# Optimization experiments

Measured on AMD Instinct MI355X. Metric: run time of the kernel, lower is better.

Reference implementation:

```python
import jax, jax.numpy as jnp
import numpy as np

N, Lq, Lk = 4, 4096, 4096
H, P = 16, 128
D = H * P  # 2048


def setup_inputs() -> dict:
    key = jax.random.key(0)
    ks = jax.random.split(key, 7)
    s = 1.0 / np.sqrt(D).astype(np.float32)
    query = jax.random.normal(ks[0], (N, Lq, D), jnp.float32)
    key_t = jax.random.normal(ks[1], (N, Lk, D), jnp.float32)
    Wq = jax.random.normal(ks[2], (D, D), jnp.float32) * s
    Wk = jax.random.normal(ks[3], (D, D), jnp.float32) * s
    Wv = jax.random.normal(ks[4], (D, D), jnp.float32) * s
    query_padding_mask = jax.random.uniform(ks[5], (N, Lq)) < 0.1
    key_padding_mask = jax.random.uniform(ks[6], (N, Lk)) < 0.1
    return {"query": query, "key": key_t, "Wq": Wq, "Wk": Wk, "Wv": Wv,
            "query_padding_mask": query_padding_mask,
            "key_padding_mask": key_padding_mask}


def reference(query, key, Wq, Wk, Wv, query_padding_mask, key_padding_mask):
    n, lq, _ = query.shape
    lk = key.shape[1]
    # torch.nn.Linear(bias=False): y = x @ W^T; split into heads -> (N,H,L,P)
    q = (query @ Wq.T).reshape(n, lq, H, P).transpose(0, 2, 1, 3)
    k = (key @ Wk.T).reshape(n, lk, H, P).transpose(0, 2, 1, 3)
    v = (key @ Wv.T).reshape(n, lk, H, P).transpose(0, 2, 1, 3)
    # _log_exp_kernel(x) = log(1 + exp(x)) = softplus
    pq = jax.nn.softplus(q)
    pk = jax.nn.softplus(k)
    # zero out padded keys so they contribute nothing to numerator/denominator
    pk = jnp.where(key_padding_mask[:, None, :, None], 0.0, pk)
    # linear attention: O(L*d^2) instead of O(L^2*d)
    kv = jnp.einsum("nhkd,nhke->nhde", pk, v)          # (N,H,P,P)
    num = jnp.einsum("nhqd,nhde->nhqe", pq, kv)        # (N,H,Lq,P)
    den = jnp.einsum("nhqd,nhd->nhq", pq, pk.sum(axis=2))[..., None]
    att = num / den
    out = att.transpose(0, 2, 1, 3).reshape(n, lq, H * P)
    # zero out padded query positions
    out = jnp.where(query_padding_mask[..., None], 0.0, out)
    return out
```

## Files before the change

### kernel.cpp

```cpp
#include <hip/hip_runtime.h>
#include <stdint.h>

typedef __attribute__((ext_vector_type(8))) short    bh8;
typedef __attribute__((ext_vector_type(4))) float    fx4;
typedef __attribute__((ext_vector_type(4))) float    f4v;
typedef unsigned short u16;
typedef __attribute__((ext_vector_type(4))) unsigned short u16x4;

#define DEV static __device__ __forceinline__

DEV u16 f2bf(float f) {
  unsigned u = __float_as_uint(f);
  u += 0x7FFFu + ((u >> 16) & 1u);
  return (u16)(u >> 16);
}
DEV float bf2f(u16 s) { return __uint_as_float(((unsigned)s) << 16); }
DEV float softplus_f(float x) { return fmaxf(x, 0.f) + log1pf(expf(-fabsf(x))); }

DEV void gload_lds16(const u16* g, u16* l) {
  __builtin_amdgcn_global_load_lds(
      (const __attribute__((address_space(1))) unsigned int*)g,
      (__attribute__((address_space(3))) unsigned int*)l, 16, 0, 0);
}
DEV void stage2(const u16* s, u16* d) {
  gload_lds16(s, d);
  gload_lds16(s + 131072, d + 4096);
}

__global__ __launch_bounds__(256) void k_cvt(const float* __restrict__ in,
                                             u16* __restrict__ out, int n4) {
  int i = blockIdx.x * 256 + threadIdx.x;
  int stride = gridDim.x * 256;
  for (; i < n4; i += stride) {
    f4v v = ((const f4v*)in)[i];
    u16x4 o;
    o.x = f2bf(v.x); o.y = f2bf(v.y); o.z = f2bf(v.z); o.w = f2bf(v.w);
    ((u16x4*)out)[i] = o;
  }
}


#define MM(a, b, c) __builtin_amdgcn_mfma_f32_16x16x32_bf16(a, b, c, 0, 0, 0)
#define LD(BASE, RR, KS) \
  (*(const bh8*)&lsg[(BASE) + (RR) * 64 + ((((KS) * 32) + ko8) ^ swz)])

#define DECLQ(Q)                                                          \
  fx4 acc##Q##00 = {}, acc##Q##01 = {}, acc##Q##10 = {}, acc##Q##11 = {}, \
      acc##Q##20 = {}, acc##Q##21 = {}, acc##Q##30 = {}, acc##Q##31 = {}

#define DECLFRAGS                                                         \
  bh8 a_00 = {}, a_01 = {}, a_10 = {}, a_11 = {},                         \
      a_20 = {}, a_21 = {}, a_30 = {}, a_31 = {};                         \
  bh8 b0_00 = {}, b0_01 = {}, b0_10 = {}, b0_11 = {};                     \
  bh8 b1_00 = {}, b1_01 = {}, b1_10 = {}, b1_11 = {};

#define WV6 asm volatile("s_waitcnt vmcnt(6)");
#define WV2 asm volatile("s_waitcnt vmcnt(2)");

#define LDA4(AB, KS)                                                     \
  a_0##KS = LD(AB, arow0,      KS); a_1##KS = LD(AB, arow0 + 16, KS);    \
  a_2##KS = LD(AB, arow0 + 32, KS); a_3##KS = LD(AB, arow0 + 48, KS);

#define LDB2(BN, BB, KS)                                                 \
  b##BN##_0##KS = LD(BB, brow0,      KS);                                \
  b##BN##_1##KS = LD(BB, brow0 + 16, KS);

#define MFMA8(Q, BN, KS)                                                 \
  acc##Q##00 = MM(a_0##KS, b##BN##_0##KS, acc##Q##00);                   \
  acc##Q##01 = MM(a_0##KS, b##BN##_1##KS, acc##Q##01);                   \
  acc##Q##10 = MM(a_1##KS, b##BN##_0##KS, acc##Q##10);                   \
  acc##Q##11 = MM(a_1##KS, b##BN##_1##KS, acc##Q##11);                   \
  acc##Q##20 = MM(a_2##KS, b##BN##_0##KS, acc##Q##20);                   \
  acc##Q##21 = MM(a_2##KS, b##BN##_1##KS, acc##Q##21);                   \
  acc##Q##30 = MM(a_3##KS, b##BN##_0##KS, acc##Q##30);                   \
  acc##Q##31 = MM(a_3##KS, b##BN##_1##KS, acc##Q##31);

#define PH4(MFMAS, WAIT, ...) {                 \
  __VA_ARGS__                                   \
  __builtin_amdgcn_s_barrier();                 \
  __builtin_amdgcn_s_setprio(1);                \
  MFMAS                                         \
  __builtin_amdgcn_s_setprio(0);                \
  WAIT                                          \
  __builtin_amdgcn_s_barrier();                 \
}

#define STE(AC, EL, JOFF) {                                                   \
  float v = AC.EL;                                                            \
  if (EPI >= 1) v = softplus_f(v);                                            \
  if (EPI == 2) { if (mask[gi0 + JOFF]) v = 0.f; }                            \
  C[(size_t)(gi0 + JOFF) * 2048 + gj] = f2bf(v);                              \
}
#define ST1(AC, QR, QC, MI, NI) {                                             \
  int gi0 = bm0 + (QR) * 128 + wr * 64 + (MI) * 16 + (lane >> 4) * 4;         \
  int gj  = bn0 + (QC) * 128 + wc * 32 + (NI) * 16 + l15;                     \
  STE(AC, x, 0) STE(AC, y, 1) STE(AC, z, 2) STE(AC, w, 3)                     \
}
#define EPIQ(Q, QR, QC)                                                       \
  ST1(acc##Q##00, QR, QC, 0, 0) ST1(acc##Q##01, QR, QC, 0, 1)                 \
  ST1(acc##Q##10, QR, QC, 1, 0) ST1(acc##Q##11, QR, QC, 1, 1)                 \
  ST1(acc##Q##20, QR, QC, 2, 0) ST1(acc##Q##21, QR, QC, 2, 1)                 \
  ST1(acc##Q##30, QR, QC, 3, 0) ST1(acc##Q##31, QR, QC, 3, 1)

template <int EPI>
__global__ __launch_bounds__(512, 2) void k_gemm256(
    const u16* __restrict__ A, const u16* __restrict__ B, u16* __restrict__ C,
    const int* __restrict__ mask) {
  extern __shared__ u16 lsg[];
  int tid = threadIdx.x, lane = tid & 63, wid = tid >> 6;
  int xcd = blockIdx.x & 7, i = blockIdx.x >> 3;
  int bm0 = (xcd * 8 + (i & 7)) << 8;
  int bn0 = (i >> 3) << 8;
  int wr = wid >> 2, wc = wid & 3;
  int l15 = lane & 15, ko8 = (lane >> 4) * 8;
  int swz = (l15 & 7) << 3;
  int arow0 = wr * 64 + l15, brow0 = wc * 32 + l15;
  int lr = lane >> 3, cg = (lane & 7) ^ lr;
  const u16* srcA = A + (size_t)(bm0 + wid * 8 + lr) * 2048 + cg * 8;
  const u16* srcB = B + (size_t)(bn0 + wid * 8 + lr) * 2048 + cg * 8;
  u16* lsu = lsg + wid * 512;

  DECLQ(0); DECLQ(1); DECLQ(2); DECLQ(3);
  DECLFRAGS

  stage2(srcA, lsu + 0);
  stage2(srcB, lsu + 16384);
  stage2(srcB + 262144, lsu + 24576);
  stage2(srcA + 262144, lsu + 8192);
  asm volatile("s_waitcnt vmcnt(0)");
  __builtin_amdgcn_s_barrier();

  for (int it = 0; it < 16; it++) {
    int tO = 2 * it + 1;
    int tE = (2 * it + 2) & 31;
    PH4(MFMA8(0, 0, 0) MFMA8(1, 1, 0) MFMA8(0, 0, 1) MFMA8(1, 1, 1), WV6,
        LDA4(0, 0) LDB2(0, 16384, 0) LDB2(1, 24576, 0)
        LDA4(0, 1) LDB2(0, 16384, 1) LDB2(1, 24576, 1)
        stage2(srcA + tO * 64, lsu + 32768);
        stage2(srcB + tO * 64, lsu + 49152);
        stage2(srcB + 262144 + tO * 64, lsu + 57344);)
    PH4(MFMA8(2, 0, 0) MFMA8(3, 1, 0) MFMA8(2, 0, 1) MFMA8(3, 1, 1), WV2,
        LDA4(8192, 0) LDA4(8192, 1)
        stage2(srcA + 262144 + tO * 64, lsu + 40960);)
    PH4(MFMA8(0, 0, 0) MFMA8(1, 1, 0) MFMA8(0, 0, 1) MFMA8(1, 1, 1), WV6,
        LDA4(32768, 0) LDB2(0, 49152, 0) LDB2(1, 57344, 0)
        LDA4(32768, 1) LDB2(0, 49152, 1) LDB2(1, 57344, 1)
        stage2(srcA + tE * 64, lsu + 0);
        stage2(srcB + tE * 64, lsu + 16384);
        stage2(srcB + 262144 + tE * 64, lsu + 24576);)
    PH4(MFMA8(2, 0, 0) MFMA8(3, 1, 0) MFMA8(2, 0, 1) MFMA8(3, 1, 1), WV2,
        LDA4(40960, 0) LDA4(40960, 1)
        stage2(srcA + 262144 + tE * 64, lsu + 8192);)
  }

  EPIQ(0, 0, 0)
  EPIQ(1, 0, 1)
  EPIQ(2, 1, 0)
  EPIQ(3, 1, 1)
}

__global__ __launch_bounds__(256, 2) void k_kv2(const u16* __restrict__ pk,
                                                const u16* __restrict__ v,
                                                float* __restrict__ part,
                                                float* __restrict__ spart) {
  int nh = blockIdx.x >> 3, slab = blockIdx.x & 7;
  int n = nh >> 4, h = nh & 15;
  __shared__ u16 lsA[128 * 32];
  __shared__ u16 lsB[128 * 32];
  __shared__ float redS[32][128];
  int tid = threadIdx.x, lane = tid & 63, wid = tid >> 6;
  int wr = wid >> 1, wc = wid & 1;
  int kk = tid >> 3;
  int dg = (tid & 7) * 16;
  size_t rowbase = ((size_t)(n * 4096 + slab * 512) + kk) * 2048 + h * 128 + dg;
  int r = lane & 15, ko = (lane >> 4) * 8;
  fx4 acc[4][4] = {};
  float sA[16];
#pragma unroll
  for (int i = 0; i < 16; i++) sA[i] = 0.f;
  for (int k0 = 0; k0 < 512; k0 += 32) {
    __syncthreads();
    bh8 a0 = *(const bh8*)(pk + rowbase + (size_t)k0 * 2048);
    bh8 a1 = *(const bh8*)(pk + rowbase + (size_t)k0 * 2048 + 8);
    bh8 b0 = *(const bh8*)(v + rowbase + (size_t)k0 * 2048);
    bh8 b1 = *(const bh8*)(v + rowbase + (size_t)k0 * 2048 + 8);
#pragma unroll
    for (int i = 0; i < 8; i++) {
      sA[i] += bf2f((u16)a0[i]);
      sA[8 + i] += bf2f((u16)a1[i]);
    }
#pragma unroll
    for (int i = 0; i < 8; i++) {
      lsA[(dg + i) * 32 + kk] = (u16)a0[i];
      lsA[(dg + 8 + i) * 32 + kk] = (u16)a1[i];
      lsB[(dg + i) * 32 + kk] = (u16)b0[i];
      lsB[(dg + 8 + i) * 32 + kk] = (u16)b1[i];
    }
    __syncthreads();
    bh8 af[4], bfr[4];
#pragma unroll
    for (int mi = 0; mi < 4; mi++)
      af[mi] = *(const bh8*)&lsA[(wr * 64 + mi * 16 + r) * 32 + ko];
#pragma unroll
    for (int ni = 0; ni < 4; ni++)
      bfr[ni] = *(const bh8*)&lsB[(wc * 64 + ni * 16 + r) * 32 + ko];
#pragma unroll
    for (int mi = 0; mi < 4; mi++)
#pragma unroll
      for (int ni = 0; ni < 4; ni++)
        acc[mi][ni] = __builtin_amdgcn_mfma_f32_16x16x32_bf16(af[mi], bfr[ni],
                                                              acc[mi][ni], 0, 0, 0);
  }
#pragma unroll
  for (int mi = 0; mi < 4; mi++)
#pragma unroll
    for (int ni = 0; ni < 4; ni++)
#pragma unroll
      for (int j = 0; j < 4; j++) {
        int d = wr * 64 + mi * 16 + (lane >> 4) * 4 + j;
        int e = wc * 64 + ni * 16 + (lane & 15);
        part[(size_t)blockIdx.x * 16384 + e * 128 + d] = acc[mi][ni][j];
      }
#pragma unroll
  for (int i = 0; i < 16; i++) redS[kk][dg + i] = sA[i];
  __syncthreads();
  if (tid < 128) {
    float s = 0.f;
#pragma unroll
    for (int p = 0; p < 32; p++) s += redS[p][tid];
    spart[blockIdx.x * 128 + tid] = s;
  }
}

__global__ __launch_bounds__(256) void k_red(const float* __restrict__ part,
                                             const float* __restrict__ spart,
                                             u16* __restrict__ kvT,
                                             float* __restrict__ sb) {
  int nh = blockIdx.x, tid = threadIdx.x;
  for (int i = tid; i < 16384; i += 256) {
    float s = 0.f;
#pragma unroll
    for (int sl = 0; sl < 8; sl++) s += part[(size_t)(nh * 8 + sl) * 16384 + i];
    kvT[(size_t)nh * 16384 + i] = f2bf(s);
  }
  if (tid < 128) {
    float s = 0.f;
#pragma unroll
    for (int sl = 0; sl < 8; sl++) s += spart[(nh * 8 + sl) * 128 + tid];
    sb[nh * 128 + tid] = s;
  }
}

__global__ __launch_bounds__(256, 2) void k_att(
    const u16* __restrict__ pq, const u16* __restrict__ kvT,
    const float* __restrict__ s, const int* __restrict__ qmask,
    float* __restrict__ out) {
  int b = blockIdx.x;
  int lt = b & 31, h = (b >> 5) & 15, nb = b >> 9;
  int l0 = lt * 128;
  __shared__ u16 lsQ[128 * 128];
  __shared__ u16 lsKV[128 * 128];
  __shared__ float lsS[128];
  __shared__ float lsDen[128];
  int tid = threadIdx.x, lane = tid & 63, wid = tid >> 6;

  int row = tid >> 1, part = tid & 1;
  const u16* gq = pq + ((size_t)(nb * 4096 + l0 + row)) * 2048 + h * 128 + part * 64;
  const u16* gk = kvT + ((size_t)(nb * 16 + h) * 128 + row) * 128 + part * 64;
  int sw = (row & 7) << 3;
#pragma unroll
  for (int j = 0; j < 8; j++) {
    bh8 vq = *(const bh8*)(gq + j * 8);
    bh8 vk = *(const bh8*)(gk + j * 8);
    int ci = (part * 64 + j * 8) ^ sw;
    *(bh8*)&lsQ[row * 128 + ci] = vq;
    *(bh8*)&lsKV[row * 128 + ci] = vk;
  }
  if (tid < 128) lsS[tid] = s[(nb * 16 + h) * 128 + tid];
  __syncthreads();

  if (tid < 128) {
    int rr = tid, swr = (rr & 7) << 3;
    float dsum = 0.f;
    for (int dd = 0; dd < 128; dd++) {
      int d = (dd + rr) & 127;
      dsum += bf2f(lsQ[rr * 128 + (d ^ swr)]) * lsS[d];
    }
    lsDen[rr] = dsum;
  }
  __syncthreads();

  int wr = wid >> 1, wc = wid & 1;
  int r = lane & 15, ko = (lane >> 4) * 8;
  fx4 acc[4][4] = {};
#pragma unroll
  for (int ks = 0; ks < 4; ks++) {
    bh8 af[4], bfr[4];
#pragma unroll
    for (int mi = 0; mi < 4; mi++) {
      int rw = wr * 64 + mi * 16 + r;
      af[mi] = *(const bh8*)&lsQ[rw * 128 + ((ks * 32 + ko) ^ ((rw & 7) << 3))];
    }
#pragma unroll
    for (int ni = 0; ni < 4; ni++) {
      int rw = wc * 64 + ni * 16 + r;
      bfr[ni] = *(const bh8*)&lsKV[rw * 128 + ((ks * 32 + ko) ^ ((rw & 7) << 3))];
    }
#pragma unroll
    for (int mi = 0; mi < 4; mi++)
#pragma unroll
      for (int ni = 0; ni < 4; ni++)
        acc[mi][ni] = __builtin_amdgcn_mfma_f32_16x16x32_bf16(af[mi], bfr[ni],
                                                              acc[mi][ni], 0, 0, 0);
  }
#pragma unroll
  for (int mi = 0; mi < 4; mi++)
#pragma unroll
    for (int ni = 0; ni < 4; ni++)
#pragma unroll
      for (int j = 0; j < 4; j++) {
        int li = wr * 64 + mi * 16 + (lane >> 4) * 4 + j;
        int e = wc * 64 + ni * 16 + (lane & 15);
        int l = l0 + li;
        float v = qmask[nb * 4096 + l] ? 0.f : acc[mi][ni][j] / lsDen[li];
        out[((size_t)(nb * 4096 + l)) * 2048 + h * 128 + e] = v;
      }
}

extern "C" void kernel_launch(void* const* d_in, const int* in_sizes, int n_in,
                              void* d_out, int out_size, void* d_ws, size_t ws_size,
                              hipStream_t stream) {
  const float* query = (const float*)d_in[0];
  const float* key   = (const float*)d_in[1];
  const float* Wq    = (const float*)d_in[2];
  const float* Wk    = (const float*)d_in[3];
  const float* Wv    = (const float*)d_in[4];
  const int* qmask   = (const int*)d_in[5];
  const int* kmask   = (const int*)d_in[6];
  float* out = (float*)d_out;
  char* ws = (char*)d_ws;

  u16* qb   = (u16*)(ws + 0);
  u16* kb   = (u16*)(ws + 67108864ull);
  u16* Wqb  = (u16*)(ws + 134217728ull);
  u16* Wkb  = (u16*)(ws + 142606336ull);
  u16* Wvb  = (u16*)(ws + 150994944ull);
  u16* pq   = (u16*)(ws + 159383552ull);
  u16* kvT  = (u16*)(ws + 226492416ull);
  float* sb = (float*)(ws + 228589568ull);
  float* kvpart = (float*)(ws + 0);
  float* spart  = (float*)(ws + 33554432ull);
  u16* pk = (u16*)d_out;
  u16* vb = (u16*)d_out + 33554432ull;

  k_cvt<<<2048, 256, 0, stream>>>(query, qb, 33554432 / 4);
  k_cvt<<<2048, 256, 0, stream>>>(key, kb, 33554432 / 4);
  k_cvt<<<512, 256, 0, stream>>>(Wq, Wqb, 4194304 / 4);
  k_cvt<<<512, 256, 0, stream>>>(Wk, Wkb, 4194304 / 4);
  k_cvt<<<512, 256, 0, stream>>>(Wv, Wvb, 4194304 / 4);

  k_gemm256<1><<<512, 512, 131072, stream>>>(qb, Wqb, pq, nullptr);
  k_gemm256<2><<<512, 512, 131072, stream>>>(kb, Wkb, pk, kmask);
  k_gemm256<0><<<512, 512, 131072, stream>>>(kb, Wvb, vb, nullptr);

  k_kv2<<<512, 256, 0, stream>>>(pk, vb, kvpart, spart);
  k_red<<<64, 256, 0, stream>>>(kvpart, spart, kvT, sb);
  k_att<<<2048, 256, 0, stream>>>(pq, kvT, sb, qmask, out);
}
```

Baseline: 743.7 us.

## Restructure GEMM main loop into one barrier per K-tile with full prefetch

Replaces the four-phase loop, which had two barriers per phase and partial vmcnt waits, with one region per K-tile. Each region issues all global-to-LDS prefetches for the next tile first, reads the current tile's fragments, runs all 32 MFMAs per quadrant pair with the second A-half loads interleaved, then waits on vmcnt(0) and issues a single barrier. The aim is to cut barrier count and synchronisation stalls between waves. The cost is that all LDS fragment reads now precede the MFMAs with less interleaving, which raises register pressure and may expose LDS latency.

Result: no change. 740.9 us (-0.4%).

```diff
diff --git a/kernel.cpp b/kernel.cpp
--- a/kernel.cpp
+++ b/kernel.cpp
@@ -54,9 +54,6 @@
   bh8 b0_00 = {}, b0_01 = {}, b0_10 = {}, b0_11 = {};                     \
   bh8 b1_00 = {}, b1_01 = {}, b1_10 = {}, b1_11 = {};
 
-#define WV6 asm volatile("s_waitcnt vmcnt(6)");
-#define WV2 asm volatile("s_waitcnt vmcnt(2)");
-
 #define LDA4(AB, KS)                                                     \
   a_0##KS = LD(AB, arow0,      KS); a_1##KS = LD(AB, arow0 + 16, KS);    \
   a_2##KS = LD(AB, arow0 + 32, KS); a_3##KS = LD(AB, arow0 + 48, KS);
@@ -75,14 +72,21 @@
   acc##Q##30 = MM(a_3##KS, b##BN##_0##KS, acc##Q##30);                   \
   acc##Q##31 = MM(a_3##KS, b##BN##_1##KS, acc##Q##31);
 
-#define PH4(MFMAS, WAIT, ...) {                 \
-  __VA_ARGS__                                   \
-  __builtin_amdgcn_s_barrier();                 \
-  __builtin_amdgcn_s_setprio(1);                \
-  MFMAS                                         \
-  __builtin_amdgcn_s_setprio(0);                \
-  WAIT                                          \
-  __builtin_amdgcn_s_barrier();                 \
+#define KREGION(ABASE, BBASE, DA, DB, SA, SB) {                          \
+  stage2(SA,            lsu + (DA));                                     \
+  stage2((SA) + 262144, lsu + (DA) + 8192);                              \
+  stage2(SB,            lsu + (DB));                                     \
+  stage2((SB) + 262144, lsu + (DB) + 8192);                              \
+  LDA4(ABASE, 0) LDA4(ABASE, 1)                                          \
+  LDB2(0, BBASE, 0) LDB2(0, BBASE, 1)                                    \
+  LDB2(1, (BBASE) + 8192, 0) LDB2(1, (BBASE) + 8192, 1)                  \
+  __builtin_amdgcn_s_setprio(1);                                         \
+  MFMA8(0, 0, 0) MFMA8(0, 0, 1) MFMA8(1, 1, 0) MFMA8(1, 1, 1)            \
+  LDA4((ABASE) + 8192, 0) LDA4((ABASE) + 8192, 1)                        \
+  MFMA8(2, 0, 0) MFMA8(2, 0, 1) MFMA8(3, 1, 0) MFMA8(3, 1, 1)            \
+  __builtin_amdgcn_s_setprio(0);                                         \
+  asm volatile("s_waitcnt vmcnt(0)");                                    \
+  __builtin_amdgcn_s_barrier();                                          \
 }
 
 #define STE(AC, EL, JOFF) {                                                   \
@@ -123,34 +127,21 @@
   DECLQ(0); DECLQ(1); DECLQ(2); DECLQ(3);
   DECLFRAGS
 
-  stage2(srcA, lsu + 0);
-  stage2(srcB, lsu + 16384);
+  stage2(srcA,          lsu + 0);
+  stage2(srcA + 262144, lsu + 8192);
+  stage2(srcB,          lsu + 16384);
   stage2(srcB + 262144, lsu + 24576);
-  stage2(srcA + 262144, lsu + 8192);
   asm volatile("s_waitcnt vmcnt(0)");
   __builtin_amdgcn_s_barrier();
 
   for (int it = 0; it < 16; it++) {
-    int tO = 2 * it + 1;
-    int tE = (2 * it + 2) & 31;
-    PH4(MFMA8(0, 0, 0) MFMA8(1, 1, 0) MFMA8(0, 0, 1) MFMA8(1, 1, 1), WV6,
-        LDA4(0, 0) LDB2(0, 16384, 0) LDB2(1, 24576, 0)
-        LDA4(0, 1) LDB2(0, 16384, 1) LDB2(1, 24576, 1)
-        stage2(srcA + tO * 64, lsu + 32768);
-        stage2(srcB + tO * 64, lsu + 49152);
-        stage2(srcB + 262144 + tO * 64, lsu + 57344);)
-    PH4(MFMA8(2, 0, 0) MFMA8(3, 1, 0) MFMA8(2, 0, 1) MFMA8(3, 1, 1), WV2,
-        LDA4(8192, 0) LDA4(8192, 1)
-        stage2(srcA + 262144 + tO * 64, lsu + 40960);)
-    PH4(MFMA8(0, 0, 0) MFMA8(1, 1, 0) MFMA8(0, 0, 1) MFMA8(1, 1, 1), WV6,
-        LDA4(32768, 0) LDB2(0, 49152, 0) LDB2(1, 57344, 0)
-        LDA4(32768, 1) LDB2(0, 49152, 1) LDB2(1, 57344, 1)
-        stage2(srcA + tE * 64, lsu + 0);
-        stage2(srcB + tE * 64, lsu + 16384);
-        stage2(srcB + 262144 + tE * 64, lsu + 24576);)
-    PH4(MFMA8(2, 0, 0) MFMA8(3, 1, 0) MFMA8(2, 0, 1) MFMA8(3, 1, 1), WV2,
-        LDA4(40960, 0) LDA4(40960, 1)
-        stage2(srcA + 262144 + tE * 64, lsu + 8192);)
+    const u16* sA1 = srcA + (2 * it + 1) * 64;
+    const u16* sB1 = srcB + (2 * it + 1) * 64;
+    int t2 = (2 * it + 2) & 31;
+    const u16* sA2 = srcA + t2 * 64;
+    const u16* sB2 = srcB + t2 * 64;
+    KREGION(0,     16384, 32768, 49152, sA1, sB1)
+    KREGION(32768, 49152, 0,     16384, sA2, sB2)
   }
 
   EPIQ(0, 0, 0)
```
